# Kernel optimization log

Hardware: AMD Instinct MI355X
Metric: run time of the kernel (lower is better)

Reference implementation:

```python
import jax, jax.numpy as jnp
import numpy as np

IN_SIZE = 64
NUM_FEATURES = 32
NUM_HEADS = 8
EPS = 1e-5


def setup_inputs() -> dict:
    key = jax.random.key(0)
    ks = jax.random.split(key, 12)
    D, F, Hh = IN_SIZE, NUM_FEATURES, NUM_HEADS
    M = Hh * F  # MLP width = num_heads * num_features
    s = 0.05
    return {
        "x": jax.random.normal(ks[0], (2, D, 48, 48), dtype=jnp.float32),
        # stacked per-head projection weights, stored [in, out]
        "Wq": jax.random.normal(ks[1], (Hh, D, F), dtype=jnp.float32) * s,
        "bq": jax.random.normal(ks[2], (Hh, F), dtype=jnp.float32) * s,
        "Wk": jax.random.normal(ks[3], (Hh, D, F), dtype=jnp.float32) * s,
        "bk": jax.random.normal(ks[4], (Hh, F), dtype=jnp.float32) * s,
        "Wv": jax.random.normal(ks[5], (Hh, D, F), dtype=jnp.float32) * s,
        "bv": jax.random.normal(ks[6], (Hh, F), dtype=jnp.float32) * s,
        "W1": jax.random.normal(ks[7], (M, M), dtype=jnp.float32) * s,
        "b1": jax.random.normal(ks[8], (M,), dtype=jnp.float32) * s,
        "W2": jax.random.normal(ks[9], (M, M), dtype=jnp.float32) * s,
        "b2": jax.random.normal(ks[10], (M,), dtype=jnp.float32) * s,
        "gamma": jnp.ones((M,), dtype=jnp.float32),
        "beta": jnp.zeros((M,), dtype=jnp.float32),
    }


def _inorm_lastdim(y):
    # InstanceNorm1d applied to channels-last tensor: normalizes LAST dim,
    # biased variance, eps=1e-5, no affine.
    mu = jnp.mean(y, axis=-1, keepdims=True)
    var = jnp.mean(jnp.square(y - mu), axis=-1, keepdims=True)
    return (y - mu) / jnp.sqrt(var + EPS)


def reference(x, Wq, bq, Wk, bk, Wv, bv, W1, b1, W2, b2, gamma, beta):
    N, D, H, W = x.shape
    F = NUM_FEATURES
    L = H * W
    flat = jnp.transpose(x, (0, 2, 3, 1)).reshape(N, L, D)  # [N, L, D]

    def proj(Wm, bm):  # Wm [Hh, D, F], bm [Hh, F] -> [Hh, N, L, F]
        y = jnp.einsum('nld,hdf->hnlf', flat, Wm) + bm[:, None, None, :]
        return jax.nn.relu(_inorm_lastdim(y))

    Q = proj(Wq, bq)
    K = proj(Wk, bk)
    V = proj(Wv, bv)

    scores = jnp.einsum('hnlf,hnmf->hnlm', Q, K) / jnp.sqrt(jnp.float32(F))
    # original: F.softmax(scaled) on 3D [N,L,L] -> legacy dim=1 (first L axis)
    att = jax.nn.softmax(scores, axis=2)
    A = jnp.einsum('hnlm,hnmf->hnlf', att, V)  # [Hh, N, L, F]

    heads = jnp.transpose(A, (1, 2, 0, 3)).reshape(N, L, NUM_HEADS * F)
    m = jax.nn.relu(heads @ W1 + b1)
    m = jax.nn.relu(m @ W2 + b2)
    o = _inorm_lastdim(m + heads)
    o = gamma * o + beta  # [N, L, Hh*F]
    return jnp.transpose(o, (0, 2, 1)).reshape(N, NUM_HEADS * F, H, W)
```

## Files before the change

### kernel.cpp

```cpp
#include <hip/hip_runtime.h>
#include <hip/hip_bf16.h>
#include <stdint.h>

#define L_TOT 2304
#define D_IN  64
#define NF    32
#define NH    8
#define NB    2
#define MW    256
#define CHS   8
#define NSTRIP (L_TOT/32)

constexpr float EPSV  = 1e-5f;
constexpr float SCALE2 = 0.2550351f;

typedef __bf16  bf16x8  __attribute__((ext_vector_type(8)));
typedef float   f32x16  __attribute__((ext_vector_type(16)));
typedef float   f32x4   __attribute__((ext_vector_type(4)));

union U32x4BF { uint32_t u[4]; bf16x8 v; };

static __device__ __forceinline__ uint32_t pack_bf16(float a, float b) {
    union { __bf16 h[2]; uint32_t u; } r;
    r.h[0] = (__bf16)a;
    r.h[1] = (__bf16)b;
    return r.u;
}

__global__ __launch_bounds__(256) void k_prep(
    const float* __restrict__ x,
    const float* __restrict__ Wq, const float* __restrict__ Wk, const float* __restrict__ Wv,
    const float* __restrict__ W1, const float* __restrict__ W2,
    __hip_bfloat16* __restrict__ xb, __hip_bfloat16* __restrict__ Wqkvt,
    __hip_bfloat16* __restrict__ W1t, __hip_bfloat16* __restrict__ W2t)
{
    const int job = blockIdx.x;
    const int tx = threadIdx.x & 31, ty = threadIdx.x >> 5;
    __shared__ float t[64][33];

    if (job < 128) {
        const int z = job >> 6;
        const int tt = job & 63;
        const int bi = (tt >> 3) * 32, bj = (tt & 7) * 32;
        const float* src = z ? W2 : W1;
        __hip_bfloat16* dst = z ? W2t : W1t;
        #pragma unroll
        for (int k = 0; k < 4; ++k)
            t[ty + 8 * k][tx] = src[(size_t)(bi + ty + 8 * k) * MW + bj + tx];
        __syncthreads();
        #pragma unroll
        for (int k = 0; k < 4; ++k)
            dst[(size_t)(bj + ty + 8 * k) * MW + bi + tx] =
                __float2bfloat16(t[tx][ty + 8 * k]);
        return;
    }

    const float* src;
    size_t sstride;
    __hip_bfloat16* dst;
    if (job < 152) {
        int j = job - 128;
        int mtx = j >> 3, h = j & 7;
        const float* Wm = mtx == 0 ? Wq : (mtx == 1 ? Wk : Wv);
        src = Wm + (size_t)h * D_IN * NF;
        sstride = NF;
        dst = Wqkvt + (size_t)j * NF * D_IN;
    } else {
        int i = job - 152;
        int n = i / NSTRIP, lt = i % NSTRIP;
        src = x + (size_t)n * D_IN * L_TOT + lt * 32;
        sstride = L_TOT;
        dst = xb + ((size_t)n * L_TOT + lt * 32) * D_IN;
    }
    #pragma unroll
    for (int k = 0; k < 8; ++k)
        t[ty + 8 * k][tx] = src[(size_t)(ty + 8 * k) * sstride + tx];
    __syncthreads();
    #pragma unroll
    for (int k = 0; k < 4; ++k) {
        int col = ty + 8 * k;
        #pragma unroll
        for (int j = 0; j < 2; ++j)
            dst[(size_t)col * D_IN + tx + 32 * j] = __float2bfloat16(t[tx + 32 * j][col]);
    }
}

__global__ __launch_bounds__(512) void k_proj(
    const __hip_bfloat16* __restrict__ xb, const __hip_bfloat16* __restrict__ Wqkvt,
    const float* __restrict__ bq, const float* __restrict__ bk, const float* __restrict__ bv,
    __hip_bfloat16* __restrict__ Qo, __hip_bfloat16* __restrict__ Ko,
    __hip_bfloat16* __restrict__ Vt)
{
    const int ltile = blockIdx.x;
    const int n = blockIdx.y;
    const int mtx = blockIdx.z;
    const int h = threadIdx.x >> 6;
    const int l0 = ltile * 32;
    const int lane = threadIdx.x & 63;
    const int c = lane & 31, hi = lane >> 5;
    const int hn = h * NB + n;

    const bf16x8* xp = reinterpret_cast<const bf16x8*>(
        xb + ((size_t)n * L_TOT + l0 + c) * D_IN);
    bf16x8 xf[4];
    #pragma unroll
    for (int t = 0; t < 4; ++t) xf[t] = xp[2 * t + hi];

    const float* bsp = mtx == 0 ? bq : (mtx == 1 ? bk : bv);

    const bf16x8* wp = reinterpret_cast<const bf16x8*>(
        Wqkvt + ((size_t)(mtx * NH + h) * NF + c) * D_IN);
    f32x16 acc = {};
    #pragma unroll
    for (int t = 0; t < 4; ++t)
        acc = __builtin_amdgcn_mfma_f32_32x32x16_bf16(wp[2 * t + hi], xf[t], acc, 0, 0, 0);

    float bb[16];
    #pragma unroll
    for (int g = 0; g < 4; ++g) {
        float4 t4 = *reinterpret_cast<const float4*>(&bsp[h * NF + 8 * g + 4 * hi]);
        bb[4 * g + 0] = t4.x; bb[4 * g + 1] = t4.y;
        bb[4 * g + 2] = t4.z; bb[4 * g + 3] = t4.w;
    }

    float v[16], s = 0.f, s2 = 0.f;
    #pragma unroll
    for (int r = 0; r < 16; ++r) {
        v[r] = acc[r] + bb[r];
        s += v[r]; s2 += v[r] * v[r];
    }
    s  += __shfl_xor(s, 32, 64);
    s2 += __shfl_xor(s2, 32, 64);
    float mu = s * (1.f / 32);
    float rstd = rsqrtf(s2 * (1.f / 32) - mu * mu + EPSV);
    float y[16];
    #pragma unroll
    for (int r = 0; r < 16; ++r) y[r] = fmaxf((v[r] - mu) * rstd, 0.f);

    if (mtx == 2) {
        #pragma unroll
        for (int r = 0; r < 16; ++r) {
            int f = (r & 3) + 8 * (r >> 2) + 4 * hi;
            Vt[((size_t)(hn * NSTRIP + ltile) * NF + f) * 32 + c] = __float2bfloat16(y[r]);
        }
    } else {
        if (mtx == 0) {
            #pragma unroll
            for (int r = 0; r < 16; ++r) y[r] *= SCALE2;
        }
        uint32_t pk[8];
        #pragma unroll
        for (int q = 0; q < 8; ++q) pk[q] = pack_bf16(y[2 * q], y[2 * q + 1]);
        uint32_t rr[4];
        #pragma unroll
        for (int j = 0; j < 4; ++j)
            rr[j] = (uint32_t)__shfl_xor((int)(hi ? pk[j] : pk[4 + j]), 32, 64);
        uint32_t row[8];
        if (hi == 0) {
            row[0] = pk[0]; row[1] = pk[1]; row[2] = rr[0]; row[3] = rr[1];
            row[4] = pk[2]; row[5] = pk[3]; row[6] = rr[2]; row[7] = rr[3];
        } else {
            row[0] = rr[0]; row[1] = rr[1]; row[2] = pk[4]; row[3] = pk[5];
            row[4] = rr[2]; row[5] = rr[3]; row[6] = pk[6]; row[7] = pk[7];
        }
        __hip_bfloat16* dst = (mtx == 0 ? Qo : Ko)
            + ((size_t)hn * L_TOT + l0 + c) * NF + hi * 16;
        reinterpret_cast<uint4*>(dst)[0] = make_uint4(row[0], row[1], row[2], row[3]);
        reinterpret_cast<uint4*>(dst)[1] = make_uint4(row[4], row[5], row[6], row[7]);
    }
}

__global__ __launch_bounds__(256) void k_stats(
    const __hip_bfloat16* __restrict__ Qb, const __hip_bfloat16* __restrict__ Kb,
    float* __restrict__ zpart)
{
    const int w = threadIdx.x >> 6;
    const int strip = blockIdx.x * 4 + w;
    const int hn = blockIdx.y;
    const int chunk = blockIdx.z;
    const int lane = threadIdx.x & 63;
    const int c = lane & 31, hi = lane >> 5;

    const bf16x8* kp = reinterpret_cast<const bf16x8*>(
        Kb + ((size_t)hn * L_TOT + strip * 32 + c) * NF);
    const bf16x8 kb0 = kp[hi];
    const bf16x8 kb1 = kp[2 + hi];

    float z0 = 0.f, z1 = 0.f, z2 = 0.f, z3 = 0.f;

    for (int it = 0; it < (L_TOT / 32) / CHS; ++it) {
        const int l0 = (chunk * ((L_TOT / 32) / CHS) + it) * 32;
        const bf16x8* qp = reinterpret_cast<const bf16x8*>(
            Qb + ((size_t)hn * L_TOT + l0 + c) * NF);
        f32x16 s16 = {};
        s16 = __builtin_amdgcn_mfma_f32_32x32x16_bf16(qp[hi], kb0, s16, 0, 0, 0);
        s16 = __builtin_amdgcn_mfma_f32_32x32x16_bf16(qp[2 + hi], kb1, s16, 0, 0, 0);
        #pragma unroll
        for (int r = 0; r < 4; ++r) z0 += exp2f(s16[r]);
        #pragma unroll
        for (int r = 4; r < 8; ++r) z1 += exp2f(s16[r]);
        #pragma unroll
        for (int r = 8; r < 12; ++r) z2 += exp2f(s16[r]);
        #pragma unroll
        for (int r = 12; r < 16; ++r) z3 += exp2f(s16[r]);
    }
    float Z = (z0 + z1) + (z2 + z3);
    Z += __shfl_xor(Z, 32, 64);
    if (hi == 0)
        zpart[((size_t)chunk * 16 + hn) * L_TOT + strip * 32 + c] = Z;
}

__global__ __launch_bounds__(256) void k_norm(
    const float* __restrict__ zpart, __hip_bfloat16* __restrict__ Vt)
{
    const int strip = blockIdx.x, hn = blockIdx.y;
    __shared__ float zs[CHS][32];
    __shared__ float zinv_s[32];

    const int cc = threadIdx.x >> 5, p = threadIdx.x & 31;
    zs[cc][p] = zpart[((size_t)cc * 16 + hn) * L_TOT + strip * 32 + p];
    __syncthreads();
    if (threadIdx.x < 32) {
        float Z = 0.f;
        #pragma unroll
        for (int k = 0; k < CHS; ++k) Z += zs[k][threadIdx.x];
        zinv_s[threadIdx.x] = 1.f / Z;
    }
    __syncthreads();

    const int f = threadIdx.x >> 3, mg = (threadIdx.x & 7) * 4;
    __hip_bfloat16* pv = Vt + ((size_t)(hn * NSTRIP + strip) * NF + f) * 32 + mg;
    uint2* p2v = reinterpret_cast<uint2*>(pv);
    union { uint2 u2; __bf16 h[4]; } in, outv;
    in.u2 = *p2v;
    outv.h[0] = (__bf16)((float)in.h[0] * zinv_s[mg + 0]);
    outv.h[1] = (__bf16)((float)in.h[1] * zinv_s[mg + 1]);
    outv.h[2] = (__bf16)((float)in.h[2] * zinv_s[mg + 2]);
    outv.h[3] = (__bf16)((float)in.h[3] * zinv_s[mg + 3]);
    *p2v = outv.u2;
}

static __device__ __forceinline__ void make_pfrags(
    const f32x16& s16, int hi, U32x4BF& fragP0, U32x4BF& fragP1)
{
    float p[16];
    #pragma unroll
    for (int r = 0; r < 16; ++r) p[r] = exp2f(s16[r]);

    uint32_t wp[8];
    #pragma unroll
    for (int q = 0; q < 8; ++q) wp[q] = pack_bf16(p[2 * q], p[2 * q + 1]);

    uint32_t sendA = hi ? wp[0] : wp[2];
    uint32_t sendB = hi ? wp[1] : wp[3];
    uint32_t rA = (uint32_t)__shfl_xor((int)sendA, 32, 64);
    uint32_t rB = (uint32_t)__shfl_xor((int)sendB, 32, 64);
    fragP0.u[0] = hi ? rA    : wp[0];
    fragP0.u[1] = hi ? rB    : wp[1];
    fragP0.u[2] = hi ? wp[2] : rA;
    fragP0.u[3] = hi ? wp[3] : rB;
    uint32_t sendC = hi ? wp[4] : wp[6];
    uint32_t sendD = hi ? wp[5] : wp[7];
    uint32_t rC = (uint32_t)__shfl_xor((int)sendC, 32, 64);
    uint32_t rD = (uint32_t)__shfl_xor((int)sendD, 32, 64);
    fragP1.u[0] = hi ? rC    : wp[4];
    fragP1.u[1] = hi ? rD    : wp[5];
    fragP1.u[2] = hi ? wp[6] : rC;
    fragP1.u[3] = hi ? wp[7] : rD;
}

__global__ __launch_bounds__(512) void k_apply(
    const __hip_bfloat16* __restrict__ Qb, const __hip_bfloat16* __restrict__ Kb,
    const __hip_bfloat16* __restrict__ Vt,
    float* __restrict__ partA)
{
    const int w = threadIdx.x >> 6;
    const int l0 = blockIdx.x * 64;
    const int hn = blockIdx.y;
    const int lane = threadIdx.x & 63;
    const int c = lane & 31, hi = lane >> 5;

    const bf16x8* qp0 = reinterpret_cast<const bf16x8*>(
        Qb + ((size_t)hn * L_TOT + l0 + c) * NF);
    const bf16x8* qp1 = reinterpret_cast<const bf16x8*>(
        Qb + ((size_t)hn * L_TOT + l0 + 32 + c) * NF);
    const bf16x8 qa0 = qp0[hi], qa1 = qp0[2 + hi];
    const bf16x8 qc0 = qp1[hi], qc1 = qp1[2 + hi];

    f32x16 acc0 = {}, acc1 = {};

    #pragma unroll 3
    for (int it = 0; it < NSTRIP / 8; ++it) {
        const int st = w * (NSTRIP / 8) + it;
        const bf16x8* kp = reinterpret_cast<const bf16x8*>(
            Kb + ((size_t)hn * L_TOT + st * 32 + c) * NF);
        const bf16x8 kf0 = kp[hi], kf1 = kp[2 + hi];
        const bf16x8* vp = reinterpret_cast<const bf16x8*>(
            Vt + ((size_t)(hn * NSTRIP + st) * NF + c) * 32);
        const bf16x8 vf0 = vp[hi], vf1 = vp[2 + hi];

        {
            f32x16 s16 = {};
            s16 = __builtin_amdgcn_mfma_f32_32x32x16_bf16(kf0, qa0, s16, 0, 0, 0);
            s16 = __builtin_amdgcn_mfma_f32_32x32x16_bf16(kf1, qa1, s16, 0, 0, 0);
            U32x4BF fragP0, fragP1;
            make_pfrags(s16, hi, fragP0, fragP1);
            acc0 = __builtin_amdgcn_mfma_f32_32x32x16_bf16(fragP0.v, vf0, acc0, 0, 0, 0);
            acc0 = __builtin_amdgcn_mfma_f32_32x32x16_bf16(fragP1.v, vf1, acc0, 0, 0, 0);
        }
        {
            f32x16 s16 = {};
            s16 = __builtin_amdgcn_mfma_f32_32x32x16_bf16(kf0, qc0, s16, 0, 0, 0);
            s16 = __builtin_amdgcn_mfma_f32_32x32x16_bf16(kf1, qc1, s16, 0, 0, 0);
            U32x4BF fragP0, fragP1;
            make_pfrags(s16, hi, fragP0, fragP1);
            acc1 = __builtin_amdgcn_mfma_f32_32x32x16_bf16(fragP0.v, vf0, acc1, 0, 0, 0);
            acc1 = __builtin_amdgcn_mfma_f32_32x32x16_bf16(fragP1.v, vf1, acc1, 0, 0, 0);
        }
    }

    __shared__ float red[8][16][64];
    const int n = hn & 1, h = hn >> 1;

    #pragma unroll
    for (int r = 0; r < 16; ++r) red[w][r][lane] = acc0[r];
    __syncthreads();
    {
        float* outp = partA + ((size_t)(n * L_TOT + l0)) * MW + h * NF + c;
        #pragma unroll
        for (int j = 0; j < 2; ++j) {
            const int r = 2 * w + j;
            float sv = 0.f;
            #pragma unroll
            for (int k = 0; k < 8; ++k) sv += red[k][r][lane];
            const int row = (r & 3) + 8 * (r >> 2) + 4 * hi;
            outp[(size_t)row * MW] = sv;
        }
    }
    __syncthreads();
    #pragma unroll
    for (int r = 0; r < 16; ++r) red[w][r][lane] = acc1[r];
    __syncthreads();
    {
        float* outp = partA + ((size_t)(n * L_TOT + l0 + 32)) * MW + h * NF + c;
        #pragma unroll
        for (int j = 0; j < 2; ++j) {
            const int r = 2 * w + j;
            float sv = 0.f;
            #pragma unroll
            for (int k = 0; k < 8; ++k) sv += red[k][r][lane];
            const int row = (r & 3) + 8 * (r >> 2) + 4 * hi;
            outp[(size_t)row * MW] = sv;
        }
    }
}

__global__ __launch_bounds__(512) void k_mlp(
    const float* __restrict__ partA,
    const __hip_bfloat16* __restrict__ W1t, const float* __restrict__ b1,
    const __hip_bfloat16* __restrict__ W2t, const float* __restrict__ b2,
    const float* __restrict__ gamma, const float* __restrict__ beta,
    float* __restrict__ out)
{
    const int blk = blockIdx.x;
    const int n  = blk / (L_TOT / 16);
    const int l0 = (blk % (L_TOT / 16)) * 16;
    const int tid = threadIdx.x;
    const int w = tid >> 6, lane = tid & 63;
    const int ar = lane & 15;
    const int kg = lane >> 4;
    const int n0 = w * 32;

    __shared__ __align__(16) char smem[50176];
    float (*hsf)[MW] = reinterpret_cast<float (*)[MW]>(smem);
    __hip_bfloat16 (*hA)[264]  = reinterpret_cast<__hip_bfloat16 (*)[264]>(smem + 16384);
    __hip_bfloat16 (*msb)[264] = reinterpret_cast<__hip_bfloat16 (*)[264]>(smem + 24832);
    float (*ys)[MW] = reinterpret_cast<float (*)[MW]>(smem + 33280);
    float (*rs)[4]  = reinterpret_cast<float (*)[4]>(smem + 49664);
    float (*rs2)[4] = reinterpret_cast<float (*)[4]>(smem + 49920);

    for (int idx = tid; idx < 16 * MW; idx += 512) {
        int r = idx >> 8, i = idx & 255;
        float v = partA[((size_t)n * L_TOT + l0 + r) * MW + i];
        hsf[r][i] = v;
        hA[r][i] = __float2bfloat16(v);
    }
    __syncthreads();

    f32x4 acc0 = {}, acc1 = {};
    {
        const __hip_bfloat16* B0p = W1t + (size_t)(n0 + ar) * MW + kg * 8;
        const __hip_bfloat16* B1p = W1t + (size_t)(n0 + 16 + ar) * MW + kg * 8;
        #pragma unroll
        for (int ks = 0; ks < 8; ++ks) {
            bf16x8 a  = *reinterpret_cast<const bf16x8*>(&hA[ar][ks * 32 + kg * 8]);
            bf16x8 b0 = *reinterpret_cast<const bf16x8*>(B0p + ks * 32);
            bf16x8 b1v = *reinterpret_cast<const bf16x8*>(B1p + ks * 32);
            acc0 = __builtin_amdgcn_mfma_f32_16x16x32_bf16(a, b0, acc0, 0, 0, 0);
            acc1 = __builtin_amdgcn_mfma_f32_16x16x32_bf16(a, b1v, acc1, 0, 0, 0);
        }
    }
    {
        const float bb0 = b1[n0 + ar], bb1 = b1[n0 + 16 + ar];
        #pragma unroll
        for (int r = 0; r < 4; ++r) {
            int row = kg * 4 + r;
            msb[row][n0 + ar]      = __float2bfloat16(fmaxf(acc0[r] + bb0, 0.f));
            msb[row][n0 + 16 + ar] = __float2bfloat16(fmaxf(acc1[r] + bb1, 0.f));
        }
    }
    __syncthreads();

    f32x4 a20 = {}, a21 = {};
    {
        const __hip_bfloat16* B0p = W2t + (size_t)(n0 + ar) * MW + kg * 8;
        const __hip_bfloat16* B1p = W2t + (size_t)(n0 + 16 + ar) * MW + kg * 8;
        #pragma unroll
        for (int ks = 0; ks < 8; ++ks) {
            bf16x8 a  = *reinterpret_cast<const bf16x8*>(&msb[ar][ks * 32 + kg * 8]);
            bf16x8 b0 = *reinterpret_cast<const bf16x8*>(B0p + ks * 32);
            bf16x8 b1v = *reinterpret_cast<const bf16x8*>(B1p + ks * 32);
            a20 = __builtin_amdgcn_mfma_f32_16x16x32_bf16(a, b0, a20, 0, 0, 0);
            a21 = __builtin_amdgcn_mfma_f32_16x16x32_bf16(a, b1v, a21, 0, 0, 0);
        }
    }
    {
        const float bb0 = b2[n0 + ar], bb1 = b2[n0 + 16 + ar];
        #pragma unroll
        for (int r = 0; r < 4; ++r) {
            int row = kg * 4 + r;
            ys[row][n0 + ar]      = fmaxf(a20[r] + bb0, 0.f) + hsf[row][n0 + ar];
            ys[row][n0 + 16 + ar] = fmaxf(a21[r] + bb1, 0.f) + hsf[row][n0 + 16 + ar];
        }
    }
    __syncthreads();

    const int col = tid & 255;
    const int half = tid >> 8;
    const int wid = (tid >> 6) & 3;
    float vv[8];
    #pragma unroll
    for (int r = 0; r < 8; ++r) {
        float v = ys[half * 8 + r][col];
        vv[r] = v;
        float s = v, s2 = v * v;
        #pragma unroll
        for (int o = 32; o >= 1; o >>= 1) { s += __shfl_xor(s, o, 64); s2 += __shfl_xor(s2, o, 64); }
        if (lane == 0) { rs[half * 8 + r][wid] = s; rs2[half * 8 + r][wid] = s2; }
    }
    __syncthreads();
    const float g = gamma[col], be = beta[col];
    float ov[8];
    #pragma unroll
    for (int r = 0; r < 8; ++r) {
        int row = half * 8 + r;
        float s  = rs[row][0]  + rs[row][1]  + rs[row][2]  + rs[row][3];
        float s2 = rs2[row][0] + rs2[row][1] + rs2[row][2] + rs2[row][3];
        float mu  = s  * (1.f / MW);
        float var = s2 * (1.f / MW) - mu * mu;
        ov[r] = g * ((vv[r] - mu) * rsqrtf(var + EPSV)) + be;
    }
    float* ob = out + ((size_t)n * MW + col) * L_TOT + l0 + half * 8;
    reinterpret_cast<float4*>(ob)[0] = make_float4(ov[0], ov[1], ov[2], ov[3]);
    reinterpret_cast<float4*>(ob)[1] = make_float4(ov[4], ov[5], ov[6], ov[7]);
}

extern "C" void kernel_launch(void* const* d_in, const int* in_sizes, int n_in,
                              void* d_out, int out_size, void* d_ws, size_t ws_size,
                              hipStream_t stream) {
    const float* x  = (const float*)d_in[0];
    const float* Wq = (const float*)d_in[1];
    const float* bq = (const float*)d_in[2];
    const float* Wk = (const float*)d_in[3];
    const float* bk = (const float*)d_in[4];
    const float* Wv = (const float*)d_in[5];
    const float* bv = (const float*)d_in[6];
    const float* W1 = (const float*)d_in[7];
    const float* b1 = (const float*)d_in[8];
    const float* W2 = (const float*)d_in[9];
    const float* b2 = (const float*)d_in[10];
    const float* gm = (const float*)d_in[11];
    const float* bt = (const float*)d_in[12];
    float* out = (float*)d_out;

    const size_t QKVE = (size_t)16 * L_TOT * NF;
    const size_t XBE  = (size_t)NB * L_TOT * D_IN;
    const size_t WQE  = (size_t)3 * NH * NF * D_IN;
    const size_t WTE  = (size_t)MW * MW;
    const size_t ZN = (size_t)CHS * 16 * L_TOT;

    __hip_bfloat16* Qb = (__hip_bfloat16*)d_ws;
    __hip_bfloat16* Kb = Qb + QKVE;
    __hip_bfloat16* Vt = Kb + QKVE;
    __hip_bfloat16* xb = Vt + QKVE;
    __hip_bfloat16* Wqkvt = xb + XBE;
    __hip_bfloat16* W1t = Wqkvt + WQE;
    __hip_bfloat16* W2t = W1t + WTE;
    float* zpart = (float*)(W2t + WTE);
    float* partA = zpart + ZN;

    k_prep<<<dim3(296), dim3(256), 0, stream>>>(
        x, Wq, Wk, Wv, W1, W2, xb, Wqkvt, W1t, W2t);
    k_proj<<<dim3(NSTRIP, NB, 3), dim3(512), 0, stream>>>(
        xb, Wqkvt, bq, bk, bv, Qb, Kb, Vt);
    k_stats<<<dim3(NSTRIP / 4, 16, CHS), dim3(256), 0, stream>>>(Qb, Kb, zpart);
    k_norm<<<dim3(NSTRIP, 16), dim3(256), 0, stream>>>(zpart, Vt);
    k_apply<<<dim3(NSTRIP / 2, 16), dim3(512), 0, stream>>>(Qb, Kb, Vt, partA);
    k_mlp<<<dim3(NB * (L_TOT / 16)), dim3(512), 0, stream>>>(
        partA, W1t, b1, W2t, b2, gm, bt, out);
}
```

Before: 124.7 us.

## Fold softmax normalization into apply kernel and use hardware exp2

Removes the standalone normalization kernel that rescaled V by 1/Z. Each apply block instead reduces the partial Z sums for its head into a shared 1/Z table and multiplies the probabilities by it before packing to bf16. exp2f is replaced by the amdgcn exp2 builtin. This saves a launch and a pass over V, but each block redundantly re-reads zpart and adds per-element multiplies and LDS loads in the inner loop.

After: 110.3 us (median of 3 runs). -11.5%, faster.

```diff
diff --git a/kernel.cpp b/kernel.cpp
--- a/kernel.cpp
+++ b/kernel.cpp
@@ -13,6 +13,12 @@
 
 constexpr float EPSV  = 1e-5f;
 constexpr float SCALE2 = 0.2550351f;
+
+#if __has_builtin(__builtin_amdgcn_exp2f)
+#define EXP2(x) __builtin_amdgcn_exp2f(x)
+#else
+#define EXP2(x) exp2f(x)
+#endif
 
 typedef __bf16  bf16x8  __attribute__((ext_vector_type(8)));
 typedef float   f32x16  __attribute__((ext_vector_type(16)));
@@ -196,13 +202,13 @@
         s16 = __builtin_amdgcn_mfma_f32_32x32x16_bf16(qp[hi], kb0, s16, 0, 0, 0);
         s16 = __builtin_amdgcn_mfma_f32_32x32x16_bf16(qp[2 + hi], kb1, s16, 0, 0, 0);
         #pragma unroll
-        for (int r = 0; r < 4; ++r) z0 += exp2f(s16[r]);
-        #pragma unroll
-        for (int r = 4; r < 8; ++r) z1 += exp2f(s16[r]);
-        #pragma unroll
-        for (int r = 8; r < 12; ++r) z2 += exp2f(s16[r]);
-        #pragma unroll
-        for (int r = 12; r < 16; ++r) z3 += exp2f(s16[r]);
+        for (int r = 0; r < 4; ++r) z0 += EXP2(s16[r]);
+        #pragma unroll
+        for (int r = 4; r < 8; ++r) z1 += EXP2(s16[r]);
+        #pragma unroll
+        for (int r = 8; r < 12; ++r) z2 += EXP2(s16[r]);
+        #pragma unroll
+        for (int r = 12; r < 16; ++r) z3 += EXP2(s16[r]);
     }
     float Z = (z0 + z1) + (z2 + z3);
     Z += __shfl_xor(Z, 32, 64);
@@ -210,42 +216,13 @@
         zpart[((size_t)chunk * 16 + hn) * L_TOT + strip * 32 + c] = Z;
 }
 
-__global__ __launch_bounds__(256) void k_norm(
-    const float* __restrict__ zpart, __hip_bfloat16* __restrict__ Vt)
-{
-    const int strip = blockIdx.x, hn = blockIdx.y;
-    __shared__ float zs[CHS][32];
-    __shared__ float zinv_s[32];
-
-    const int cc = threadIdx.x >> 5, p = threadIdx.x & 31;
-    zs[cc][p] = zpart[((size_t)cc * 16 + hn) * L_TOT + strip * 32 + p];
-    __syncthreads();
-    if (threadIdx.x < 32) {
-        float Z = 0.f;
-        #pragma unroll
-        for (int k = 0; k < CHS; ++k) Z += zs[k][threadIdx.x];
-        zinv_s[threadIdx.x] = 1.f / Z;
-    }
-    __syncthreads();
-
-    const int f = threadIdx.x >> 3, mg = (threadIdx.x & 7) * 4;
-    __hip_bfloat16* pv = Vt + ((size_t)(hn * NSTRIP + strip) * NF + f) * 32 + mg;
-    uint2* p2v = reinterpret_cast<uint2*>(pv);
-    union { uint2 u2; __bf16 h[4]; } in, outv;
-    in.u2 = *p2v;
-    outv.h[0] = (__bf16)((float)in.h[0] * zinv_s[mg + 0]);
-    outv.h[1] = (__bf16)((float)in.h[1] * zinv_s[mg + 1]);
-    outv.h[2] = (__bf16)((float)in.h[2] * zinv_s[mg + 2]);
-    outv.h[3] = (__bf16)((float)in.h[3] * zinv_s[mg + 3]);
-    *p2v = outv.u2;
-}
-
 static __device__ __forceinline__ void make_pfrags(
-    const f32x16& s16, int hi, U32x4BF& fragP0, U32x4BF& fragP1)
+    const f32x16& s16, const float* __restrict__ zi, int hi,
+    U32x4BF& fragP0, U32x4BF& fragP1)
 {
     float p[16];
     #pragma unroll
-    for (int r = 0; r < 16; ++r) p[r] = exp2f(s16[r]);
+    for (int r = 0; r < 16; ++r) p[r] = EXP2(s16[r]) * zi[r];
 
     uint32_t wp[8];
     #pragma unroll
@@ -271,7 +248,7 @@
 
 __global__ __launch_bounds__(512) void k_apply(
     const __hip_bfloat16* __restrict__ Qb, const __hip_bfloat16* __restrict__ Kb,
-    const __hip_bfloat16* __restrict__ Vt,
+    const __hip_bfloat16* __restrict__ Vt, const float* __restrict__ zpart,
     float* __restrict__ partA)
 {
     const int w = threadIdx.x >> 6;
@@ -279,6 +256,16 @@
     const int hn = blockIdx.y;
     const int lane = threadIdx.x & 63;
     const int c = lane & 31, hi = lane >> 5;
+
+    __shared__ float zinv_s[L_TOT];
+    for (int m = threadIdx.x; m < L_TOT; m += 512) {
+        float Z = 0.f;
+        #pragma unroll
+        for (int k = 0; k < CHS; ++k)
+            Z += zpart[((size_t)k * 16 + hn) * L_TOT + m];
+        zinv_s[m] = 1.f / Z;
+    }
+    __syncthreads();
 
     const bf16x8* qp0 = reinterpret_cast<const bf16x8*>(
         Qb + ((size_t)hn * L_TOT + l0 + c) * NF);
@@ -299,12 +286,17 @@
             Vt + ((size_t)(hn * NSTRIP + st) * NF + c) * 32);
         const bf16x8 vf0 = vp[hi], vf1 = vp[2 + hi];
 
+        float zi[16];
+        #pragma unroll
+        for (int r = 0; r < 16; ++r)
+            zi[r] = zinv_s[st * 32 + (r & 3) + 8 * (r >> 2) + 4 * hi];
+
         {
             f32x16 s16 = {};
             s16 = __builtin_amdgcn_mfma_f32_32x32x16_bf16(kf0, qa0, s16, 0, 0, 0);
             s16 = __builtin_amdgcn_mfma_f32_32x32x16_bf16(kf1, qa1, s16, 0, 0, 0);
             U32x4BF fragP0, fragP1;
-            make_pfrags(s16, hi, fragP0, fragP1);
+            make_pfrags(s16, zi, hi, fragP0, fragP1);
             acc0 = __builtin_amdgcn_mfma_f32_32x32x16_bf16(fragP0.v, vf0, acc0, 0, 0, 0);
             acc0 = __builtin_amdgcn_mfma_f32_32x32x16_bf16(fragP1.v, vf1, acc0, 0, 0, 0);
         }
@@ -313,7 +305,7 @@
             s16 = __builtin_amdgcn_mfma_f32_32x32x16_bf16(kf0, qc0, s16, 0, 0, 0);
             s16 = __builtin_amdgcn_mfma_f32_32x32x16_bf16(kf1, qc1, s16, 0, 0, 0);
             U32x4BF fragP0, fragP1;
-            make_pfrags(s16, hi, fragP0, fragP1);
+            make_pfrags(s16, zi, hi, fragP0, fragP1);
             acc1 = __builtin_amdgcn_mfma_f32_32x32x16_bf16(fragP0.v, vf0, acc1, 0, 0, 0);
             acc1 = __builtin_amdgcn_mfma_f32_32x32x16_bf16(fragP1.v, vf1, acc1, 0, 0, 0);
         }
@@ -504,8 +496,8 @@
     k_proj<<<dim3(NSTRIP, NB, 3), dim3(512), 0, stream>>>(
         xb, Wqkvt, bq, bk, bv, Qb, Kb, Vt);
     k_stats<<<dim3(NSTRIP / 4, 16, CHS), dim3(256), 0, stream>>>(Qb, Kb, zpart);
-    k_norm<<<dim3(NSTRIP, 16), dim3(256), 0, stream>>>(zpart, Vt);
-    k_apply<<<dim3(NSTRIP / 2, 16), dim3(512), 0, stream>>>(Qb, Kb, Vt, partA);
+    k_apply<<<dim3(NSTRIP / 2, 16), dim3(512), 0, stream>>>(
+        Qb, Kb, Vt, zpart, partA);
     k_mlp<<<dim3(NB * (L_TOT / 16)), dim3(512), 0, stream>>>(
         partA, W1t, b1, W2t, b2, gm, bt, out);
 }
```
